# Performance work log

Measured on AMD Instinct MI355X. Metric: run time of the kernel, lower is better.

Reference implementation:

```python
import jax, jax.numpy as jnp
import numpy as np

H, DK = 4, 64
D = H * DK              # hidden_dim = 256
D_OUT = 64
L = 2
NT, ET = 2, 3
AUTHOR, PAPER = 0, 1                 # sorted ntypes: ['author','paper']
CITES, WRITES, WRITTEN_BY = 0, 1, 2  # sorted etypes: ['cites','writes','written-by']
NA, NPAPER = 20000, 40000
E_WB, E_W, E_C = 150000, 150000, 300000
SQRT_DK = float(np.sqrt(DK))
EPS = 1e-5


def setup_inputs() -> dict:
    key = jax.random.key(0)
    ks = jax.random.split(key, 24)
    s = 1.0 / np.sqrt(D)
    return {
        "x_author": jax.random.normal(ks[0], (NA, D), jnp.float32),
        "x_paper": jax.random.normal(ks[1], (NPAPER, D), jnp.float32),
        "ew_wb": jax.random.uniform(ks[2], (E_WB,), jnp.float32),
        "ew_w": jax.random.uniform(ks[3], (E_W,), jnp.float32),
        "ew_c": jax.random.uniform(ks[4], (E_C,), jnp.float32),
        "adapt_W": jax.random.normal(ks[5], (NT, D, D), jnp.float32) * s,
        "adapt_b": jnp.zeros((NT, D), jnp.float32),
        "kW": jax.random.normal(ks[6], (L, NT, D, D), jnp.float32) * s,
        "kb": jnp.zeros((L, NT, D), jnp.float32),
        "qW": jax.random.normal(ks[7], (L, NT, D, D), jnp.float32) * s,
        "qb": jnp.zeros((L, NT, D), jnp.float32),
        "mW": jax.random.normal(ks[8], (L, NT, D, D), jnp.float32) * s,
        "mb": jnp.zeros((L, NT, D), jnp.float32),
        "aW": jax.random.normal(ks[9], (L, NT, D, D), jnp.float32) * s,
        "ab": jnp.zeros((L, NT, D), jnp.float32),
        "w_pri": jnp.ones((L, ET, H), jnp.float32),
        "w_att": jax.random.normal(ks[10], (L, ET, H, DK, DK), jnp.float32) / np.sqrt(DK),
        "w_msg": jax.random.normal(ks[11], (L, ET, H, DK, DK), jnp.float32) / np.sqrt(DK),
        "skip": jnp.ones((L, ET), jnp.float32),
        "ln_g": jnp.ones((L, NT, D), jnp.float32),
        "ln_b": jnp.zeros((L, NT, D), jnp.float32),
        "out_W": jax.random.normal(ks[12], (D, D_OUT), jnp.float32) * s,
        "out_b": jnp.zeros((D_OUT,), jnp.float32),
        "src_wb": jax.random.randint(ks[13], (E_WB,), 0, NPAPER, jnp.int32),
        "dst_wb": jax.random.randint(ks[14], (E_WB,), 0, NA, jnp.int32),
        "src_w": jax.random.randint(ks[15], (E_W,), 0, NA, jnp.int32),
        "dst_w": jax.random.randint(ks[16], (E_W,), 0, NPAPER, jnp.int32),
        "src_c": jax.random.randint(ks[17], (E_C,), 0, NPAPER, jnp.int32),
        "dst_c": jax.random.randint(ks[18], (E_C,), 0, NPAPER, jnp.int32),
    }


def _ln(x, g, b):
    mu = x.mean(-1, keepdims=True)
    var = ((x - mu) ** 2).mean(-1, keepdims=True)
    return (x - mu) * jax.lax.rsqrt(var + EPS) * g + b


def _hgt_layer(feats, rels, kW, kb, qW, qb, mW, mb, aW, ab,
               w_pri, w_att, w_msg, skip, ln_g, ln_b):
    # feats: [x_author, x_paper]; per-ntype K/Q/M projections -> [N, H, DK]
    Ns = [f.shape[0] for f in feats]
    kbase = [(feats[t] @ kW[t] + kb[t]).reshape(-1, H, DK) for t in range(NT)]
    qbase = [(feats[t] @ qW[t] + qb[t]).reshape(-1, H, DK) for t in range(NT)]
    mbase = [(feats[t] @ mW[t] + mb[t]).reshape(-1, H, DK) for t in range(NT)]
    aggs = {}
    for (st, e, dt, src, dst, ew) in rels:
        k = jnp.einsum('nhd,hde->nhe', kbase[st], w_att[e])
        m = jnp.einsum('nhd,hde->nhe', mbase[st], w_msg[e])
        score = (qbase[dt][dst] * k[src]).sum(-1) * w_pri[e] / SQRT_DK  # [E, H]
        attn = jax.nn.sigmoid(score) * ew[:, None]
        msg = m[src] * attn[:, :, None]                                 # [E, H, DK]
        aggs[e] = jax.ops.segment_sum(msg, dst, num_segments=Ns[dt])
    # cross_reducer='mean': mean over relation aggregates per dst ntype
    t_author = aggs[WRITTEN_BY].reshape(Ns[AUTHOR], D)
    t_paper = ((aggs[WRITES] + aggs[CITES]) * 0.5).reshape(Ns[PAPER], D)
    new = []
    for nid, t in ((AUTHOR, t_author), (PAPER, t_paper)):
        alpha = jax.nn.sigmoid(skip[nid])  # skip indexed by n_id (as in source)
        tr = t @ aW[nid] + ab[nid]
        o = tr * alpha + feats[nid] * (1.0 - alpha)
        new.append(_ln(o, ln_g[nid], ln_b[nid]))
    return new


def _forward(x_author, x_paper, ew_wb, ew_w, ew_c,
             adapt_W, adapt_b, kW, kb, qW, qb, mW, mb, aW, ab,
             w_pri, w_att, w_msg, skip, ln_g, ln_b, out_W, out_b,
             src_wb, dst_wb, src_w, dst_w, src_c, dst_c):
    feats = [
        jax.nn.gelu(x_author @ adapt_W[AUTHOR] + adapt_b[AUTHOR], approximate=False),
        jax.nn.gelu(x_paper @ adapt_W[PAPER] + adapt_b[PAPER], approximate=False),
    ]
    rels = [
        (PAPER, WRITTEN_BY, AUTHOR, src_wb, dst_wb, ew_wb),
        (AUTHOR, WRITES, PAPER, src_w, dst_w, ew_w),
        (PAPER, CITES, PAPER, src_c, dst_c, ew_c),
    ]
    for l in range(L):
        feats = _hgt_layer(feats, rels, kW[l], kb[l], qW[l], qb[l], mW[l], mb[l],
                           aW[l], ab[l], w_pri[l], w_att[l], w_msg[l], skip[l],
                           ln_g[l], ln_b[l])
    return feats[PAPER] @ out_W + out_b  # out_key = 'paper'


def reference(x_author, x_paper, ew_wb, ew_w, ew_c,
              adapt_W, adapt_b, kW, kb, qW, qb, mW, mb, aW, ab,
              w_pri, w_att, w_msg, skip, ln_g, ln_b, out_W, out_b,
              src_wb, dst_wb, src_w, dst_w, src_c, dst_c):
    return _forward(x_author, x_paper, ew_wb, ew_w, ew_c,
                    adapt_W, adapt_b, kW, kb, qW, qb, mW, mb, aW, ab,
                    w_pri, w_att, w_msg, skip, ln_g, ln_b, out_W, out_b,
                    src_wb, dst_wb, src_w, dst_w, src_c, dst_c)
```

## Files before the change

### kernel.cpp

```cpp
#include <hip/hip_runtime.h>
#include <hip/hip_bf16.h>
#include <math.h>

using bf16 = __hip_bfloat16;

typedef __attribute__((ext_vector_type(8))) short short8;
typedef __attribute__((ext_vector_type(4))) float float4v;

static constexpr int kNA  = 20000;
static constexpr int kNP  = 40000;
static constexpr int kEWB = 150000;
static constexpr int kEW  = 150000;
static constexpr int kEC  = 300000;

static constexpr int kNSeg = 21;
static constexpr int kSegN[kNSeg] = {
  150000, 150000, 300000,
  131072, 512,
  262144, 1024,
  262144, 1024,
  262144, 1024,
  262144, 1024,
  24,
  98304, 98304,
  6, 1024, 1024,
  16384, 64
};
static constexpr size_t kOff(int s) {
  size_t o = 0;
  for (int i = 0; i < s; ++i) o += (size_t)kSegN[i];
  return o;
}
static constexpr size_t kCanonTotal = kOff(kNSeg);

struct CanonArgs {
  const void* src[kNSeg];
  int n[kNSeg];
  unsigned dstOff[kNSeg];
};
struct TransArgs {
  const bf16* src[10];
  bf16* dst[10];
};
struct GemmDesc {
  const short* wt;
  const bf16* bias;
  const void* A;
  void* c;
  int ldc;
  int coff;
  int act;
  int otype;
  int M;
  int ntiles;
};
struct MultiDesc { GemmDesc d[10]; };
struct ScanArgs {
  int* deg[3];
  int* offs[3];
  int* bsums;
  int N[3];
};
struct HistArgs {
  const int* dst[3];
  int* cnt[3];
  int E[3];
};
struct ScatArgs {
  const int* dst[3];
  const int* src[3];
  const bf16* ew[3];
  int* cur[3];
  int* srcs[3];
  bf16* ews[3];
  int E[3];
};
struct GatherDesc {
  const bf16* q;
  const bf16* km;
  const int* srcs;
  const bf16* ews;
  const int* offs;
  const bf16* pri;
  bf16* agg;
  int Nd;
  int addPrev;
  float scale;
};

__device__ __forceinline__ float toF(float x) { return x; }
__device__ __forceinline__ float toF(bf16 x)  { return __bfloat162float(x); }
__device__ __forceinline__ float bits2f(unsigned short b) {
  unsigned int u = ((unsigned int)b) << 16;
  return __uint_as_float(u);
}
__device__ __forceinline__ float sigmoidf_(float x) { return 1.0f / (1.0f + expf(-x)); }
__device__ __forceinline__ float gelu_exact(float x) {
  return 0.5f * x * (1.0f + erff(x * 0.70710678118654752f));
}

__global__ __launch_bounds__(256) void detect_dtype(
    const unsigned* __restrict__ x, unsigned* __restrict__ flags)
{
  __shared__ int cnt;
  if (threadIdx.x == 0) cnt = 0;
  __syncthreads();
  unsigned w = x[threadIdx.x];
  unsigned e = (w >> 7) & 0xFFu;
  if (e >= 110u && e <= 140u) atomicAdd(&cnt, 1);
  __syncthreads();
  if (threadIdx.x == 0) {
    flags[0] = (cnt >= 128) ? 1u : 0u;
    flags[1] = 1u;
  }
}

__global__ __launch_bounds__(256) void canon_kernel(
    CanonArgs a, bf16* __restrict__ dst, const unsigned* __restrict__ flags)
{
  const int s = blockIdx.y;
  const int i = blockIdx.x * 256 + threadIdx.x;
  if (i >= a.n[s]) return;
  bf16 v;
  if (flags[0]) v = ((const bf16*)a.src[s])[i];
  else          v = __float2bfloat16(((const float*)a.src[s])[i]);
  dst[a.dstOff[s] + i] = v;
}

__global__ __launch_bounds__(256) void transpose_w(TransArgs ta)
{
  const int m = blockIdx.z;
  const short* src = (const short*)ta.src[m];
  short* dst = (short*)ta.dst[m];
  const int k0 = blockIdx.x * 64, n0 = blockIdx.y * 64;
  __shared__ short tile[64][65];
  const int tx = threadIdx.x & 63, ty = threadIdx.x >> 6;
  for (int i = ty; i < 64; i += 4)
    tile[i][tx] = src[(size_t)(k0 + i) * 256 + n0 + tx];
  __syncthreads();
  for (int i = ty; i < 64; i += 4)
    dst[(size_t)(n0 + i) * 256 + k0 + tx] = tile[tx][i];
}

__global__ __launch_bounds__(256) void csr_hist(HistArgs h)
{
  const int rel = blockIdx.y;
  const int i = blockIdx.x * 256 + threadIdx.x;
  if (i < h.E[rel]) atomicAdd(&h.cnt[rel][h.dst[rel][i]], 1);
}

__global__ __launch_bounds__(256) void scan_l1(ScanArgs a)
{
  const int rel = blockIdx.y;
  const int N = a.N[rel];
  const int t = threadIdx.x;
  const int lane = t & 63;
  const int wid = t >> 6;
  const int i0 = blockIdx.x * 2048 + t * 8;
  const int* deg = a.deg[rel];
  int v[8];
  int T = 0;
  #pragma unroll
  for (int j = 0; j < 8; ++j) {
    v[j] = (i0 + j < N) ? deg[i0 + j] : 0;
    T += v[j];
  }
  int incl = T;
  #pragma unroll
  for (int off = 1; off < 64; off <<= 1) {
    const int u = __shfl_up(incl, off);
    if (lane >= off) incl += u;
  }
  __shared__ int wsum[4];
  if (lane == 63) wsum[wid] = incl;
  __syncthreads();
  int woff = 0;
  #pragma unroll
  for (int wp = 0; wp < 4; ++wp) if (wp < wid) woff += wsum[wp];
  int run = woff + incl - T;
  int* offs = a.offs[rel];
  #pragma unroll
  for (int j = 0; j < 8; ++j) {
    if (i0 + j < N) offs[i0 + j] = run;
    run += v[j];
  }
  if (t == 0)
    a.bsums[rel * 32 + blockIdx.x] = wsum[0] + wsum[1] + wsum[2] + wsum[3];
}

__global__ __launch_bounds__(64) void scan_l2(int* __restrict__ bsums,
                                              int* __restrict__ totals)
{
  const int rel = blockIdx.x;
  const int lane = threadIdx.x;
  const int v = (lane < 32) ? bsums[rel * 32 + lane] : 0;
  int incl = v;
  #pragma unroll
  for (int off = 1; off < 64; off <<= 1) {
    const int u = __shfl_up(incl, off);
    if (lane >= off) incl += u;
  }
  if (lane < 32) bsums[rel * 32 + lane] = incl - v;
  if (lane == 63) totals[rel] = incl;
}

__global__ __launch_bounds__(256) void scan_l3(ScanArgs a,
                                               const int* __restrict__ totals)
{
  const int rel = blockIdx.y;
  const int N = a.N[rel];
  const int i0 = blockIdx.x * 2048 + threadIdx.x * 8;
  const int boff = a.bsums[rel * 32 + blockIdx.x];
  int* offs = a.offs[rel];
  int* cur = a.deg[rel];
  #pragma unroll
  for (int j = 0; j < 8; ++j) {
    const int idx = i0 + j;
    if (idx < N) {
      const int o = offs[idx] + boff;
      offs[idx] = o;
      cur[idx] = o;
    }
  }
  if (blockIdx.x == 0 && threadIdx.x == 0) offs[N] = totals[rel];
}

__global__ __launch_bounds__(256) void csr_scatter(ScatArgs s)
{
  const int rel = blockIdx.y;
  const int i = blockIdx.x * 256 + threadIdx.x;
  if (i >= s.E[rel]) return;
  const int p = atomicAdd(&s.cur[rel][s.dst[rel][i]], 1);
  s.srcs[rel][p] = s.src[rel][i];
  s.ews[rel][p]  = s.ew[rel][i];
}

__global__ __launch_bounds__(256) void combine_weights(
    const bf16* __restrict__ Wbig, const bf16* __restrict__ bbig,
    const bf16* __restrict__ wsm, bf16* __restrict__ KMT,
    bf16* __restrict__ kmb, int noff)
{
  const int blk = blockIdx.y;
  const int rc  = blockIdx.x;
  const int h = blk & 3;
  const int le = blk >> 2;
  const int e = le % 3;
  const int l = le / 3;
  const int st = (e == 1) ? 0 : 1;

  const short* Wsrc = (const short*)(Wbig + (size_t)(l * 2 + st) * 65536);
  const bf16*  bsrc = bbig + (size_t)(l * 2 + st) * 256;
  const short* wm   = (const short*)(wsm + ((size_t)(l * 3 + e) * 4 + h) * 4096);
  short* outT = (short*)(KMT + (size_t)(l * 3 + e) * 512 * 256);
  bf16* outb  = kmb + (size_t)(l * 3 + e) * 512;

  __shared__ short w[64][72];
  __shared__ short As[32][72];
  __shared__ short ot[64][40];

  const int t = threadIdx.x;
  {
    const int base = t * 16;
    const int r0 = base >> 6, c0 = base & 63;
    *(short8*)&w[r0][c0]     = *(const short8*)&wm[base];
    *(short8*)&w[r0][c0 + 8] = *(const short8*)&wm[base + 8];
  }
  {
    const int row = t >> 3;
    const int kc = (t & 7) * 8;
    *(short8*)&As[row][kc] =
        *(const short8*)&Wsrc[(size_t)(rc * 32 + row) * 256 + h * 64 + kc];
  }
  __syncthreads();

  const int j   = t & 63;
  const int sub = t >> 6;
  float accv[8] = {};
  #pragma unroll
  for (int d = 0; d < 64; ++d) {
    const float wd = bits2f((unsigned short)w[d][j]);
    #pragma unroll
    for (int r8 = 0; r8 < 8; ++r8)
      accv[r8] += bits2f((unsigned short)As[sub * 8 + r8][d]) * wd;
  }
  #pragma unroll
  for (int r8 = 0; r8 < 8; ++r8) {
    union { bf16 h; short s; } cv;
    cv.h = __float2bfloat16(accv[r8]);
    ot[j][sub * 8 + r8] = cv.s;
  }

  if (rc == 0 && t < 64) {
    float acc = 0.f;
    #pragma unroll
    for (int d = 0; d < 64; ++d)
      acc += toF(bsrc[h * 64 + d]) * bits2f((unsigned short)w[d][t]);
    outb[h * 64 + t + noff] = __float2bfloat16(acc);
  }
  __syncthreads();
  {
    const int nn = t >> 2;
    const int kx = (t & 3) * 8;
    short8 v;
    #pragma unroll
    for (int x = 0; x < 8; ++x) v[x] = ot[nn][kx + x];
    *(short8*)&outT[(size_t)(h * 64 + nn + noff) * 256 + rc * 32 + kx] = v;
  }
}

__global__ __launch_bounds__(256, 4) void mfma_gemm128(
    const unsigned* __restrict__ aflag, MultiDesc md, int nslab)
{
  __shared__ short As[128][72];
  __shared__ short Bs[128][72];
  const int lid = blockIdx.x;
  const int grp = lid / (8 * nslab);
  const int rem = lid - grp * 8 * nslab;
  const int slab = rem >> 3;
  const int tx = grp * 8 + (rem & 7);
  const GemmDesc d = md.d[slab];
  if (tx >= d.ntiles) return;
  const bool abf = (*aflag != 0u);
  const int M = d.M;
  const int t = threadIdx.x;
  const int bm = tx * 128;
  const int lane = t & 63;
  const int wid  = t >> 6;
  const int wm = (wid >> 1) * 64;
  const int wn = (wid & 1) * 64;
  const int col16 = lane & 15;
  const int quad  = lane >> 4;
  const int rr = t >> 3;
  const int kk = (t & 7) * 8;

  float4v acc[4][4];
  #pragma unroll
  for (int mi = 0; mi < 4; ++mi)
    #pragma unroll
    for (int ni = 0; ni < 4; ++ni) acc[mi][ni] = (float4v){0.f, 0.f, 0.f, 0.f};

  for (int k0 = 0; k0 < 256; k0 += 64) {
    #pragma unroll
    for (int it = 0; it < 4; ++it) {
      const int row = it * 32 + rr;
      const int grow = bm + row;
      short8 v = (short8){0, 0, 0, 0, 0, 0, 0, 0};
      if (grow < M) {
        if (abf) {
          v = *(const short8*)((const short*)d.A + (size_t)grow * 256 + k0 + kk);
        } else {
          const float* ap = (const float*)d.A + (size_t)grow * 256 + k0 + kk;
          #pragma unroll
          for (int j = 0; j < 8; ++j) {
            union { bf16 h; short s; } cv;
            cv.h = __float2bfloat16(ap[j]);
            v[j] = cv.s;
          }
        }
      }
      *(short8*)&As[row][kk] = v;
    }
    #pragma unroll
    for (int it = 0; it < 4; ++it) {
      const int n = it * 32 + rr;
      *(short8*)&Bs[n][kk] = *(const short8*)&d.wt[(size_t)n * 256 + k0 + kk];
    }
    __syncthreads();

    #pragma unroll
    for (int ks = 0; ks < 64; ks += 32) {
      short8 bfr[4];
      #pragma unroll
      for (int ni = 0; ni < 4; ++ni)
        bfr[ni] = *(const short8*)&Bs[wn + ni * 16 + col16][ks + quad * 8];
      #pragma unroll
      for (int mi = 0; mi < 4; ++mi) {
        const short8 afr = *(const short8*)&As[wm + mi * 16 + col16][ks + quad * 8];
        #pragma unroll
        for (int ni = 0; ni < 4; ++ni)
          acc[mi][ni] = __builtin_amdgcn_mfma_f32_16x16x32_bf16(afr, bfr[ni], acc[mi][ni], 0, 0, 0);
      }
    }
    __syncthreads();
  }

  #pragma unroll
  for (int ni = 0; ni < 4; ++ni) {
    const int col = wn + ni * 16 + col16;
    const float bc = toF(d.bias[col]);
    const int gcol = d.coff + col;
    #pragma unroll
    for (int mi = 0; mi < 4; ++mi) {
      #pragma unroll
      for (int r = 0; r < 4; ++r) {
        const int row = bm + wm + mi * 16 + quad * 4 + r;
        if (row < M) {
          float v = acc[mi][ni][r] + bc;
          if (d.act == 1) v = gelu_exact(v);
          const size_t idx = (size_t)row * d.ldc + gcol;
          if (d.otype == 0) ((bf16*)d.c)[idx] = __float2bfloat16(v);
          else              ((float*)d.c)[idx] = v;
        }
      }
    }
  }
}

__global__ __launch_bounds__(256) void gather_fused(
    GatherDesc da, GatherDesc db, int blocksA)
{
  const GatherDesc d = (blockIdx.x < (unsigned)blocksA) ? da : db;
  const int bidx = (blockIdx.x < (unsigned)blocksA) ? blockIdx.x
                                                    : blockIdx.x - blocksA;
  const int lane = threadIdx.x & 63;
  const int wid  = threadIdx.x >> 6;
  const int node = bidx * 4 + wid;
  if (node >= d.Nd) return;
  const int h  = lane >> 5;
  const int sl = lane & 31;
  const float prih = toF(d.pri[sl >> 3]);

  union B8 { uint4 u; unsigned short s[8]; };
  B8 qv;
  qv.u = ((const uint4*)(d.q + (size_t)node * 256))[sl];
  float qf[8];
  #pragma unroll
  for (int j = 0; j < 8; ++j) qf[j] = bits2f(qv.s[j]);

  float acc[8] = {};
  const int beg = d.offs[node], end = d.offs[node + 1];
  for (int idx = beg + h; idx < end; idx += 2) {
    const int s = d.srcs[idx];
    const float w = toF(d.ews[idx]);
    B8 kb;
    kb.u = ((const uint4*)(d.km + (size_t)s * 512))[sl];
    float dot = 0.f;
    #pragma unroll
    for (int j = 0; j < 8; ++j) dot += qf[j] * bits2f(kb.s[j]);
    dot += __shfl_xor(dot, 1);
    dot += __shfl_xor(dot, 2);
    dot += __shfl_xor(dot, 4);
    const float a = w * sigmoidf_(dot * prih * 0.125f);
    B8 mb;
    mb.u = ((const uint4*)(d.km + (size_t)s * 512 + 256))[sl];
    #pragma unroll
    for (int j = 0; j < 8; ++j) acc[j] += bits2f(mb.s[j]) * a;
  }

  #pragma unroll
  for (int j = 0; j < 8; ++j) acc[j] += __shfl_xor(acc[j], 32);

  if (h == 0) {
    bf16* out = d.agg + (size_t)node * 256 + sl * 8;
    #pragma unroll
    for (int j = 0; j < 8; ++j) acc[j] *= d.scale;
    if (d.addPrev) {
      B8 pb;
      pb.u = *(const uint4*)out;
      #pragma unroll
      for (int j = 0; j < 8; ++j) acc[j] += bits2f(pb.s[j]);
    }
    B8 ov;
    #pragma unroll
    for (int j = 0; j < 8; ++j) {
      union { bf16 h; unsigned short u; } cv;
      cv.h = __float2bfloat16(acc[j]);
      ov.s[j] = cv.u;
    }
    *(uint4*)out = ov.u;
  }
}

__global__ __launch_bounds__(256) void skip_ln2(
    const float* __restrict__ trA, bf16* __restrict__ featA,
    const bf16* __restrict__ skA, const bf16* __restrict__ gA_, const bf16* __restrict__ bA,
    const float* __restrict__ trP, bf16* __restrict__ featP,
    const bf16* __restrict__ skP, const bf16* __restrict__ gP, const bf16* __restrict__ bP,
    int NA, int Ntot)
{
  const int lane = threadIdx.x & 63;
  const int wid  = threadIdx.x >> 6;
  int node = blockIdx.x * 4 + wid;
  if (node >= Ntot) return;
  const float* tr; bf16* feat; const bf16 *sk, *g, *b;
  if (node < NA) { tr = trA; feat = featA; sk = skA; g = gA_; b = bA; }
  else { node -= NA; tr = trP; feat = featP; sk = skP; g = gP; b = bP; }

  const float alpha = sigmoidf_(toF(*sk));
  const float4 t = ((const float4*)(tr + (size_t)node * 256))[lane];
  union B4 { uint2 u; unsigned short s[4]; };
  B4 fb;
  fb.u = ((const uint2*)(feat + (size_t)node * 256))[lane];
  float o[4];
  o[0] = t.x * alpha + bits2f(fb.s[0]) * (1.f - alpha);
  o[1] = t.y * alpha + bits2f(fb.s[1]) * (1.f - alpha);
  o[2] = t.z * alpha + bits2f(fb.s[2]) * (1.f - alpha);
  o[3] = t.w * alpha + bits2f(fb.s[3]) * (1.f - alpha);

  float sum = o[0] + o[1] + o[2] + o[3];
  #pragma unroll
  for (int off = 32; off; off >>= 1) sum += __shfl_xor(sum, off);
  const float mu = sum * (1.f / 256.f);

  float dd[4], sq = 0.f;
  #pragma unroll
  for (int j = 0; j < 4; ++j) { dd[j] = o[j] - mu; sq += dd[j] * dd[j]; }
  #pragma unroll
  for (int off = 32; off; off >>= 1) sq += __shfl_xor(sq, off);
  const float rs = rsqrtf(sq * (1.f / 256.f) + 1e-5f);

  bf16* fout = feat + (size_t)node * 256 + lane * 4;
  #pragma unroll
  for (int j = 0; j < 4; ++j) {
    float r = dd[j] * rs * toF(g[lane * 4 + j]) + toF(b[lane * 4 + j]);
    fout[j] = __float2bfloat16(r);
  }
}

__global__ __launch_bounds__(256) void out_gemm(
    const bf16* __restrict__ A, const bf16* __restrict__ W,
    const bf16* __restrict__ bias, void* __restrict__ out,
    const unsigned* __restrict__ flag, int M)
{
  __shared__ float Ws[64][64];
  const bool obf = (*flag != 0u);
  const int tid = threadIdx.x;
  const int row = blockIdx.x * 64 + (tid >> 2);
  const int c0 = (tid & 3) * 16;
  const int arow = (row < M) ? row : 0;
  const bf16* a = A + (size_t)arow * 256;
  float acc[16] = {};
  for (int k0 = 0; k0 < 256; k0 += 64) {
    for (int i = tid; i < 4096; i += 256)
      Ws[i >> 6][i & 63] = toF(W[(size_t)(k0 + (i >> 6)) * 64 + (i & 63)]);
    __syncthreads();
    for (int k = 0; k < 64; ++k) {
      const float av = toF(a[k0 + k]);
      #pragma unroll
      for (int j = 0; j < 16; ++j) acc[j] += av * Ws[k][c0 + j];
    }
    __syncthreads();
  }
  if (row < M) {
    #pragma unroll
    for (int j = 0; j < 16; ++j) {
      const float v = acc[j] + toF(bias[c0 + j]);
      const size_t idx = (size_t)row * 64 + c0 + j;
      if (obf) ((bf16*)out)[idx] = __float2bfloat16(v);
      else     ((float*)out)[idx] = v;
    }
  }
}

extern "C" void kernel_launch(void* const* d_in, const int* in_sizes, int n_in,
                              void* d_out, int out_size, void* d_ws, size_t ws_size,
                              hipStream_t stream) {
  const int* src_wb  = (const int*)d_in[23];
  const int* dst_wb  = (const int*)d_in[24];
  const int* src_w   = (const int*)d_in[25];
  const int* dst_w   = (const int*)d_in[26];
  const int* src_c   = (const int*)d_in[27];
  const int* dst_c   = (const int*)d_in[28];

  char* base = (char*)d_ws;
  unsigned* flags = (unsigned*)base;
  bf16* canon = (bf16*)(base + 256);
  char* p = base + 256 + (((size_t)kCanonTotal * 2 + 511) & ~(size_t)511);
  bf16* adWT = (bf16*)p;
  bf16* qWT  = adWT + (size_t)2 * 65536;
  bf16* aWT  = qWT  + (size_t)4 * 65536;
  bf16* KMeffT = aWT + (size_t)4 * 65536;
  bf16* kmbeT  = KMeffT + (size_t)6 * 512 * 256;
  char* pc = (char*)(((size_t)(kmbeT + 6 * 512) + 511) & ~(size_t)511);
  int* cur_wb  = (int*)pc;
  int* cur_w   = cur_wb + (kNA + 1);
  int* cur_c   = cur_w + (kNP + 1);
  int* offs_wb = cur_c + (kNP + 1);
  int* offs_w  = offs_wb + (kNA + 1);
  int* offs_c  = offs_w + (kNP + 1);
  int* srcs_wb = offs_c + (kNP + 1);
  int* srcs_w  = srcs_wb + kEWB;
  int* srcs_c  = srcs_w + kEW;
  bf16* ews_wb = (bf16*)(srcs_c + kEC);
  bf16* ews_w  = ews_wb + kEWB;
  bf16* ews_c  = ews_w + kEW;
  int* bsums   = (int*)(ews_c + kEC);
  int* totals  = bsums + 96;
  char* p2 = (char*)(((size_t)(totals + 3) + 511) & ~(size_t)511);
  bf16* fa  = (bf16*)p2;
  bf16* fp_ = fa + (size_t)kNA * 256;
  char* R   = (char*)(fp_ + (size_t)kNP * 256);
  bf16* qa   = (bf16*)R;
  bf16* qp   = qa + (size_t)kNA * 256;
  bf16* km_a = qp + (size_t)kNP * 256;
  bf16* km_p = km_a + (size_t)kNA * 512;
  float* tr_a = (float*)R;
  float* tr_p = tr_a + (size_t)kNA * 256;
  char* afterR = R + ((size_t)(kNA + kNP) * 256 + (size_t)(kNA + kNP) * 512) * sizeof(bf16);
  bf16* agg_a = (bf16*)afterR;
  bf16* agg_p = agg_a + (size_t)kNA * 256;

  const bf16* c_ew_wb = canon + kOff(0);
  const bf16* c_ew_w  = canon + kOff(1);
  const bf16* c_ew_c  = canon + kOff(2);
  const bf16* c_adW   = canon + kOff(3);
  const bf16* c_adb   = canon + kOff(4);
  const bf16* c_kW    = canon + kOff(5);
  const bf16* c_kb    = canon + kOff(6);
  const bf16* c_qW    = canon + kOff(7);
  const bf16* c_qb    = canon + kOff(8);
  const bf16* c_mW    = canon + kOff(9);
  const bf16* c_mb    = canon + kOff(10);
  const bf16* c_aW    = canon + kOff(11);
  const bf16* c_ab    = canon + kOff(12);
  const bf16* c_wpri  = canon + kOff(13);
  const bf16* c_watt  = canon + kOff(14);
  const bf16* c_wmsg  = canon + kOff(15);
  const bf16* c_skip  = canon + kOff(16);
  const bf16* c_lng   = canon + kOff(17);
  const bf16* c_lnb   = canon + kOff(18);
  const bf16* c_outW  = canon + kOff(19);
  const bf16* c_outb  = canon + kOff(20);

  const unsigned* fIn = flags + 0;
  const unsigned* f1  = flags + 1;

  detect_dtype<<<1, 256, 0, stream>>>((const unsigned*)d_in[0], flags);

  CanonArgs ca;
  for (int s = 0; s < kNSeg; ++s) { ca.n[s] = kSegN[s]; ca.dstOff[s] = (unsigned)kOff(s); }
  const int srcIdx[kNSeg] = {2,3,4, 5,6, 7,8, 9,10, 11,12, 13,14, 15, 16,17, 18,19,20, 21,22};
  for (int s = 0; s < kNSeg; ++s) ca.src[s] = d_in[srcIdx[s]];
  canon_kernel<<<dim3(1172, kNSeg), 256, 0, stream>>>(ca, canon, flags);

  TransArgs ta;
  ta.src[0] = c_adW;              ta.dst[0] = adWT;
  ta.src[1] = c_adW + 65536;      ta.dst[1] = adWT + 65536;
  for (int m = 0; m < 4; ++m) { ta.src[2 + m] = c_qW + (size_t)m * 65536; ta.dst[2 + m] = qWT + (size_t)m * 65536; }
  for (int m = 0; m < 4; ++m) { ta.src[6 + m] = c_aW + (size_t)m * 65536; ta.dst[6 + m] = aWT + (size_t)m * 65536; }
  transpose_w<<<dim3(4, 4, 10), 256, 0, stream>>>(ta);

  hipMemsetAsync(cur_wb, 0, (size_t)((kNA + 1) + 2 * (kNP + 1)) * 4, stream);
  HistArgs ha;
  ha.dst[0] = dst_wb; ha.cnt[0] = cur_wb; ha.E[0] = kEWB;
  ha.dst[1] = dst_w;  ha.cnt[1] = cur_w;  ha.E[1] = kEW;
  ha.dst[2] = dst_c;  ha.cnt[2] = cur_c;  ha.E[2] = kEC;
  csr_hist<<<dim3((kEC + 255) / 256, 3), 256, 0, stream>>>(ha);
  ScanArgs sa;
  sa.deg[0] = cur_wb;  sa.offs[0] = offs_wb; sa.N[0] = kNA;
  sa.deg[1] = cur_w;   sa.offs[1] = offs_w;  sa.N[1] = kNP;
  sa.deg[2] = cur_c;   sa.offs[2] = offs_c;  sa.N[2] = kNP;
  sa.bsums = bsums;
  scan_l1<<<dim3(32, 3), 256, 0, stream>>>(sa);
  scan_l2<<<3, 64, 0, stream>>>(bsums, totals);
  scan_l3<<<dim3(20, 3), 256, 0, stream>>>(sa, totals);
  ScatArgs sc;
  sc.dst[0] = dst_wb; sc.src[0] = src_wb; sc.ew[0] = c_ew_wb; sc.cur[0] = cur_wb;
  sc.srcs[0] = srcs_wb; sc.ews[0] = ews_wb; sc.E[0] = kEWB;
  sc.dst[1] = dst_w;  sc.src[1] = src_w;  sc.ew[1] = c_ew_w;  sc.cur[1] = cur_w;
  sc.srcs[1] = srcs_w;  sc.ews[1] = ews_w;  sc.E[1] = kEW;
  sc.dst[2] = dst_c;  sc.src[2] = src_c;  sc.ew[2] = c_ew_c;  sc.cur[2] = cur_c;
  sc.srcs[2] = srcs_c;  sc.ews[2] = ews_c;  sc.E[2] = kEC;
  csr_scatter<<<dim3((kEC + 255) / 256, 3), 256, 0, stream>>>(sc);

  combine_weights<<<dim3(8, 24), 256, 0, stream>>>(c_kW, c_kb, c_watt, KMeffT, kmbeT, 0);
  combine_weights<<<dim3(8, 24), 256, 0, stream>>>(c_mW, c_mb, c_wmsg, KMeffT, kmbeT, 256);

  const int ntA = (kNA + 127) / 128;
  const int ntP = (kNP + 127) / 128;
  auto sgrid = [](int maxnt, int nslab) {
    return dim3((unsigned)(((maxnt + 7) / 8) * 8 * nslab));
  };
  auto mkd = [](const bf16* wt, const bf16* bias, const void* A, void* c,
                int ldc, int coff, int act, int otype, int M, int ntiles) {
    GemmDesc g;
    g.wt = (const short*)wt; g.bias = bias; g.A = A; g.c = c; g.ldc = ldc;
    g.coff = coff; g.act = act; g.otype = otype; g.M = M; g.ntiles = ntiles;
    return g;
  };

  {
    MultiDesc md{};
    md.d[0] = mkd(adWT,                 c_adb,       d_in[0], fa,  256, 0,   1, 0, kNA, ntA);
    md.d[1] = mkd(adWT + 128 * 256,     c_adb + 128, d_in[0], fa,  256, 128, 1, 0, kNA, ntA);
    md.d[2] = mkd(adWT + 65536,         c_adb + 256, d_in[1], fp_, 256, 0,   1, 0, kNP, ntP);
    md.d[3] = mkd(adWT + 65536 + 128 * 256, c_adb + 384, d_in[1], fp_, 256, 128, 1, 0, kNP, ntP);
    mfma_gemm128<<<sgrid(ntP, 4), 256, 0, stream>>>(fIn, md, 4);
  }

  for (int l = 0; l < 2; ++l) {
    const bf16* qW_a = qWT + (size_t)(l * 2 + 0) * 65536;
    const bf16* qW_p = qWT + (size_t)(l * 2 + 1) * 65536;
    const bf16* qb_a = c_qb + (l * 2 + 0) * 256;
    const bf16* qb_p = c_qb + (l * 2 + 1) * 256;
    const bf16* KM_c  = KMeffT + (size_t)(l * 3 + 0) * 512 * 256;
    const bf16* KM_w  = KMeffT + (size_t)(l * 3 + 1) * 512 * 256;
    const bf16* KM_wb = KMeffT + (size_t)(l * 3 + 2) * 512 * 256;
    const bf16* kb_c  = kmbeT + (l * 3 + 0) * 512;
    const bf16* kb_w  = kmbeT + (l * 3 + 1) * 512;
    const bf16* kb_wb = kmbeT + (l * 3 + 2) * 512;

    {
      MultiDesc md{};
      md.d[0] = mkd(qW_p,             qb_p,       fp_, qp,   256, 0,   0, 0, kNP, ntP);
      md.d[1] = mkd(qW_p + 128 * 256, qb_p + 128, fp_, qp,   256, 128, 0, 0, kNP, ntP);
      for (int s = 0; s < 4; ++s)
        md.d[2 + s] = mkd(KM_c + (size_t)s * 128 * 256, kb_c + s * 128, fp_, km_p, 512, s * 128, 0, 0, kNP, ntP);
      mfma_gemm128<<<sgrid(ntP, 6), 256, 0, stream>>>(f1, md, 6);
    }
    {
      GatherDesc dc{qp, km_p, srcs_c, ews_c, offs_c, c_wpri + (l * 3 + 0) * 4,
                    agg_p, kNP, 0, 0.5f};
      GatherDesc dz{}; dz.Nd = 0;
      gather_fused<<<(kNP + 3) / 4, 256, 0, stream>>>(dc, dz, (kNP + 3) / 4);
    }
    {
      MultiDesc md{};
      md.d[0] = mkd(qW_a,             qb_a,       fa, qa,   256, 0,   0, 0, kNA, ntA);
      md.d[1] = mkd(qW_a + 128 * 256, qb_a + 128, fa, qa,   256, 128, 0, 0, kNA, ntA);
      for (int s = 0; s < 4; ++s)
        md.d[2 + s] = mkd(KM_w + (size_t)s * 128 * 256, kb_w + s * 128, fa, km_a, 512, s * 128, 0, 0, kNA, ntA);
      for (int s = 0; s < 4; ++s)
        md.d[6 + s] = mkd(KM_wb + (size_t)s * 128 * 256, kb_wb + s * 128, fp_, km_p, 512, s * 128, 0, 0, kNP, ntP);
      mfma_gemm128<<<sgrid(ntP, 10), 256, 0, stream>>>(f1, md, 10);
    }
    {
      GatherDesc dwb{qa, km_p, srcs_wb, ews_wb, offs_wb, c_wpri + (l * 3 + 2) * 4,
                     agg_a, kNA, 0, 1.f};
      GatherDesc dw{qp, km_a, srcs_w, ews_w, offs_w, c_wpri + (l * 3 + 1) * 4,
                    agg_p, kNP, 1, 0.5f};
      const int bA = (kNA + 3) / 4;
      gather_fused<<<bA + (kNP + 3) / 4, 256, 0, stream>>>(dwb, dw, bA);
    }
    {
      const bf16* aW_a = aWT + (size_t)(l * 2 + 0) * 65536;
      const bf16* aW_p = aWT + (size_t)(l * 2 + 1) * 65536;
      MultiDesc md{};
      md.d[0] = mkd(aW_a,             c_ab + (l * 2 + 0) * 256,       agg_a, tr_a, 256, 0,   0, 1, kNA, ntA);
      md.d[1] = mkd(aW_a + 128 * 256, c_ab + (l * 2 + 0) * 256 + 128, agg_a, tr_a, 256, 128, 0, 1, kNA, ntA);
      md.d[2] = mkd(aW_p,             c_ab + (l * 2 + 1) * 256,       agg_p, tr_p, 256, 0,   0, 1, kNP, ntP);
      md.d[3] = mkd(aW_p + 128 * 256, c_ab + (l * 2 + 1) * 256 + 128, agg_p, tr_p, 256, 128, 0, 1, kNP, ntP);
      mfma_gemm128<<<sgrid(ntP, 4), 256, 0, stream>>>(f1, md, 4);
    }
    skip_ln2<<<(kNA + kNP) / 4, 256, 0, stream>>>(
        tr_a, fa,  c_skip + l * 3 + 0, c_lng + (l * 2 + 0) * 256, c_lnb + (l * 2 + 0) * 256,
        tr_p, fp_, c_skip + l * 3 + 1, c_lng + (l * 2 + 1) * 256, c_lnb + (l * 2 + 1) * 256,
        kNA, kNA + kNP);
  }

  out_gemm<<<kNP / 64, 256, 0, stream>>>(fp_, c_outW, c_outb, d_out, fIn, kNP);
}
```

Before: 853.9 us.

## Merge per-layer projection GEMMs and fuse all three relation gathers into one kernel

```diff
diff --git a/kernel.cpp b/kernel.cpp
--- a/kernel.cpp
+++ b/kernel.cpp
@@ -54,7 +54,7 @@
   int M;
   int ntiles;
 };
-struct MultiDesc { GemmDesc d[10]; };
+struct MultiDesc { GemmDesc d[16]; };
 struct ScanArgs {
   int* deg[3];
   int* offs[3];
@@ -75,17 +75,16 @@
   bf16* ews[3];
   int E[3];
 };
-struct GatherDesc {
-  const bf16* q;
-  const bf16* km;
-  const int* srcs;
-  const bf16* ews;
-  const int* offs;
-  const bf16* pri;
-  bf16* agg;
-  int Nd;
-  int addPrev;
-  float scale;
+struct TriDesc {
+  const bf16* qa; const bf16* qp;
+  const bf16* km_wb;
+  const bf16* km_c;
+  const bf16* km_w;
+  const int* srcs_wb; const int* srcs_c; const int* srcs_w;
+  const bf16* ews_wb; const bf16* ews_c; const bf16* ews_w;
+  const int* offs_wb; const int* offs_c; const int* offs_w;
+  const bf16* pri_wb; const bf16* pri_c; const bf16* pri_w;
+  bf16* agg_a; bf16* agg_p;
 };
 
 __device__ __forceinline__ float toF(float x) { return x; }
@@ -406,34 +405,16 @@
   }
 }
 
-__global__ __launch_bounds__(256) void gather_fused(
-    GatherDesc da, GatherDesc db, int blocksA)
-{
-  const GatherDesc d = (blockIdx.x < (unsigned)blocksA) ? da : db;
-  const int bidx = (blockIdx.x < (unsigned)blocksA) ? blockIdx.x
-                                                    : blockIdx.x - blocksA;
-  const int lane = threadIdx.x & 63;
-  const int wid  = threadIdx.x >> 6;
-  const int node = bidx * 4 + wid;
-  if (node >= d.Nd) return;
-  const int h  = lane >> 5;
-  const int sl = lane & 31;
-  const float prih = toF(d.pri[sl >> 3]);
-
+__device__ __forceinline__ void gather_loop(
+    const float qf[8], const bf16* km, const int* srcs, const bf16* ews,
+    int beg, int end, int h, int sl, float prih, float acc[8])
+{
   union B8 { uint4 u; unsigned short s[8]; };
-  B8 qv;
-  qv.u = ((const uint4*)(d.q + (size_t)node * 256))[sl];
-  float qf[8];
-  #pragma unroll
-  for (int j = 0; j < 8; ++j) qf[j] = bits2f(qv.s[j]);
-
-  float acc[8] = {};
-  const int beg = d.offs[node], end = d.offs[node + 1];
   for (int idx = beg + h; idx < end; idx += 2) {
-    const int s = d.srcs[idx];
-    const float w = toF(d.ews[idx]);
+    const int s = srcs[idx];
+    const float w = toF(ews[idx]);
     B8 kb;
-    kb.u = ((const uint4*)(d.km + (size_t)s * 512))[sl];
+    kb.u = ((const uint4*)(km + (size_t)s * 512))[sl];
     float dot = 0.f;
     #pragma unroll
     for (int j = 0; j < 8; ++j) dot += qf[j] * bits2f(kb.s[j]);
@@ -442,32 +423,64 @@
     dot += __shfl_xor(dot, 4);
     const float a = w * sigmoidf_(dot * prih * 0.125f);
     B8 mb;
-    mb.u = ((const uint4*)(d.km + (size_t)s * 512 + 256))[sl];
+    mb.u = ((const uint4*)(km + (size_t)s * 512 + 256))[sl];
     #pragma unroll
     for (int j = 0; j < 8; ++j) acc[j] += bits2f(mb.s[j]) * a;
   }
+}
+
+__global__ __launch_bounds__(256) void tri_gather(TriDesc td, int bA)
+{
+  const bool isA = (blockIdx.x < (unsigned)bA);
+  const int bidx = isA ? blockIdx.x : blockIdx.x - bA;
+  const int lane = threadIdx.x & 63;
+  const int wid  = threadIdx.x >> 6;
+  const int node = bidx * 4 + wid;
+  const int Nd = isA ? kNA : kNP;
+  if (node >= Nd) return;
+  const int h  = lane >> 5;
+  const int sl = lane & 31;
+
+  union B8 { uint4 u; unsigned short s[8]; };
+  const bf16* q = isA ? td.qa : td.qp;
+  B8 qv;
+  qv.u = ((const uint4*)(q + (size_t)node * 256))[sl];
+  float qf[8];
+  #pragma unroll
+  for (int j = 0; j < 8; ++j) qf[j] = bits2f(qv.s[j]);
+
+  float acc[8] = {};
+  float scale;
+  bf16* aggout;
+  if (isA) {
+    gather_loop(qf, td.km_wb, td.srcs_wb, td.ews_wb,
+                td.offs_wb[node], td.offs_wb[node + 1], h, sl,
+                toF(td.pri_wb[sl >> 3]), acc);
+    scale = 1.f;
+    aggout = td.agg_a;
+  } else {
+    gather_loop(qf, td.km_c, td.srcs_c, td.ews_c,
+                td.offs_c[node], td.offs_c[node + 1], h, sl,
+                toF(td.pri_c[sl >> 3]), acc);
+    gather_loop(qf, td.km_w, td.srcs_w, td.ews_w,
+                td.offs_w[node], td.offs_w[node + 1], h, sl,
+                toF(td.pri_w[sl >> 3]), acc);
+    scale = 0.5f;
+    aggout = td.agg_p;
+  }
 
   #pragma unroll
   for (int j = 0; j < 8; ++j) acc[j] += __shfl_xor(acc[j], 32);
 
   if (h == 0) {
-    bf16* out = d.agg + (size_t)node * 256 + sl * 8;
-    #pragma unroll
-    for (int j = 0; j < 8; ++j) acc[j] *= d.scale;
-    if (d.addPrev) {
-      B8 pb;
-      pb.u = *(const uint4*)out;
-      #pragma unroll
-      for (int j = 0; j < 8; ++j) acc[j] += bits2f(pb.s[j]);
-    }
     B8 ov;
     #pragma unroll
     for (int j = 0; j < 8; ++j) {
       union { bf16 h; unsigned short u; } cv;
-      cv.h = __float2bfloat16(acc[j]);
+      cv.h = __float2bfloat16(acc[j] * scale);
       ov.s[j] = cv.u;
     }
-    *(uint4*)out = ov.u;
+    *(uint4*)(aggout + (size_t)node * 256 + sl * 8) = ov.u;
   }
 }
 
@@ -590,13 +603,14 @@
   bf16* fa  = (bf16*)p2;
   bf16* fp_ = fa + (size_t)kNA * 256;
   char* R   = (char*)(fp_ + (size_t)kNP * 256);
-  bf16* qa   = (bf16*)R;
-  bf16* qp   = qa + (size_t)kNA * 256;
-  bf16* km_a = qp + (size_t)kNP * 256;
-  bf16* km_p = km_a + (size_t)kNA * 512;
+  bf16* qa    = (bf16*)R;
+  bf16* qp    = qa + (size_t)kNA * 256;
+  bf16* km_a  = qp + (size_t)kNP * 256;
+  bf16* km_cp = km_a + (size_t)kNA * 512;
+  bf16* km_wbp= km_cp + (size_t)kNP * 512;
   float* tr_a = (float*)R;
   float* tr_p = tr_a + (size_t)kNA * 256;
-  char* afterR = R + ((size_t)(kNA + kNP) * 256 + (size_t)(kNA + kNP) * 512) * sizeof(bf16);
+  char* afterR = (char*)(km_wbp + (size_t)kNP * 512);
   bf16* agg_a = (bf16*)afterR;
   bf16* agg_p = agg_a + (size_t)kNA * 256;
 
@@ -681,11 +695,12 @@
 
   {
     MultiDesc md{};
-    md.d[0] = mkd(adWT,                 c_adb,       d_in[0], fa,  256, 0,   1, 0, kNA, ntA);
-    md.d[1] = mkd(adWT + 128 * 256,     c_adb + 128, d_in[0], fa,  256, 128, 1, 0, kNA, ntA);
-    md.d[2] = mkd(adWT + 65536,         c_adb + 256, d_in[1], fp_, 256, 0,   1, 0, kNP, ntP);
-    md.d[3] = mkd(adWT + 65536 + 128 * 256, c_adb + 384, d_in[1], fp_, 256, 128, 1, 0, kNP, ntP);
-    mfma_gemm128<<<sgrid(ntP, 4), 256, 0, stream>>>(fIn, md, 4);
+    md.d[0] = mkd(adWT,             c_adb,       d_in[0], fa, 256, 0,   1, 0, kNA, ntA);
+    md.d[1] = mkd(adWT + 128 * 256, c_adb + 128, d_in[0], fa, 256, 128, 1, 0, kNA, ntA);
+    mfma_gemm128<<<sgrid(ntA, 2), 256, 0, stream>>>(fIn, md, 2);
+    md.d[0] = mkd(adWT + 65536,             c_adb + 256, d_in[1], fp_, 256, 0,   1, 0, kNP, ntP);
+    md.d[1] = mkd(adWT + 65536 + 128 * 256, c_adb + 384, d_in[1], fp_, 256, 128, 1, 0, kNP, ntP);
+    mfma_gemm128<<<sgrid(ntP, 2), 256, 0, stream>>>(fIn, md, 2);
   }
 
   for (int l = 0; l < 2; ++l) {
@@ -702,35 +717,31 @@
 
     {
       MultiDesc md{};
-      md.d[0] = mkd(qW_p,             qb_p,       fp_, qp,   256, 0,   0, 0, kNP, ntP);
-      md.d[1] = mkd(qW_p + 128 * 256, qb_p + 128, fp_, qp,   256, 128, 0, 0, kNP, ntP);
+      md.d[0] = mkd(qW_p,             qb_p,       fp_, qp, 256, 0,   0, 0, kNP, ntP);
+      md.d[1] = mkd(qW_p + 128 * 256, qb_p + 128, fp_, qp, 256, 128, 0, 0, kNP, ntP);
       for (int s = 0; s < 4; ++s)
-        md.d[2 + s] = mkd(KM_c + (size_t)s * 128 * 256, kb_c + s * 128, fp_, km_p, 512, s * 128, 0, 0, kNP, ntP);
-      mfma_gemm128<<<sgrid(ntP, 6), 256, 0, stream>>>(f1, md, 6);
+        md.d[2 + s] = mkd(KM_c + (size_t)s * 128 * 256, kb_c + s * 128, fp_, km_cp, 512, s * 128, 0, 0, kNP, ntP);
+      md.d[6] = mkd(qW_a,             qb_a,       fa, qa, 256, 0,   0, 0, kNA, ntA);
+      md.d[7] = mkd(qW_a + 128 * 256, qb_a + 128, fa, qa, 256, 128, 0, 0, kNA, ntA);
+      for (int s = 0; s < 4; ++s)
+        md.d[8 + s] = mkd(KM_w + (size_t)s * 128 * 256, kb_w + s * 128, fa, km_a, 512, s * 128, 0, 0, kNA, ntA);
+      for (int s = 0; s < 4; ++s)
+        md.d[12 + s] = mkd(KM_wb + (size_t)s * 128 * 256, kb_wb + s * 128, fp_, km_wbp, 512, s * 128, 0, 0, kNP, ntP);
+      mfma_gemm128<<<sgrid(ntP, 16), 256, 0, stream>>>(f1, md, 16);
     }
     {
-      GatherDesc dc{qp, km_p, srcs_c, ews_c, offs_c, c_wpri + (l * 3 + 0) * 4,
-                    agg_p, kNP, 0, 0.5f};
-      GatherDesc dz{}; dz.Nd = 0;
-      gather_fused<<<(kNP + 3) / 4, 256, 0, stream>>>(dc, dz, (kNP + 3) / 4);
-    }
-    {
-      MultiDesc md{};
-      md.d[0] = mkd(qW_a,             qb_a,       fa, qa,   256, 0,   0, 0, kNA, ntA);
-      md.d[1] = mkd(qW_a + 128 * 256, qb_a + 128, fa, qa,   256, 128, 0, 0, kNA, ntA);
-      for (int s = 0; s < 4; ++s)
-        md.d[2 + s] = mkd(KM_w + (size_t)s * 128 * 256, kb_w + s * 128, fa, km_a, 512, s * 128, 0, 0, kNA, ntA);
-      for (int s = 0; s < 4; ++s)
-        md.d[6 + s] = mkd(KM_wb + (size_t)s * 128 * 256, kb_wb + s * 128, fp_, km_p, 512, s * 128, 0, 0, kNP, ntP);
-      mfma_gemm128<<<sgrid(ntP, 10), 256, 0, stream>>>(f1, md, 10);
-    }
-    {
-      GatherDesc dwb{qa, km_p, srcs_wb, ews_wb, offs_wb, c_wpri + (l * 3 + 2) * 4,
-                     agg_a, kNA, 0, 1.f};
-      GatherDesc dw{qp, km_a, srcs_w, ews_w, offs_w, c_wpri + (l * 3 + 1) * 4,
-                    agg_p, kNP, 1, 0.5f};
+      TriDesc td;
+      td.qa = qa; td.qp = qp;
+      td.km_wb = km_wbp; td.km_c = km_cp; td.km_w = km_a;
+      td.srcs_wb = srcs_wb; td.srcs_c = srcs_c; td.srcs_w = srcs_w;
+      td.ews_wb = ews_wb; td.ews_c = ews_c; td.ews_w = ews_w;
+      td.offs_wb = offs_wb; td.offs_c = offs_c; td.offs_w = offs_w;
+      td.pri_wb = c_wpri + (l * 3 + 2) * 4;
+      td.pri_c  = c_wpri + (l * 3 + 0) * 4;
+      td.pri_w  = c_wpri + (l * 3 + 1) * 4;
+      td.agg_a = agg_a; td.agg_p = agg_p;
       const int bA = (kNA + 3) / 4;
-      gather_fused<<<bA + (kNP + 3) / 4, 256, 0, stream>>>(dwb, dw, bA);
+      tri_gather<<<bA + (kNP + 3) / 4, 256, 0, stream>>>(td, bA);
     }
     {
       const bf16* aW_a = aWT + (size_t)(l * 2 + 0) * 65536;
```

After: 823.2 us. -3.6%, faster.
